# Kernel optimization log

Hardware: AMD Instinct MI355X
Metric: run time of the kernel (lower is better)

## Reference

```python
import jax, jax.numpy as jnp
import numpy as np

SIZE = 11
SIGMA = 1.5
ALPHA = 0.7
K1 = 0.01
K2 = 0.03
DATA_RANGE = 1.0
DN = ('NCDHW', 'OIDHW', 'NCDHW')


def _gauss1d():
    ax = jnp.arange(SIZE, dtype=jnp.float32) - SIZE // 2
    k = jnp.exp(-(ax ** 2) / (2.0 * SIGMA * SIGMA))
    return k / k.sum()


def _blur3d(x, k1):
    # Separable depthwise 3D gaussian blur with zero ('constant') padding.
    # Mathematically identical to the dense 11x11x11 outer-product conv3d
    # in the torch source (zero padding commutes with separable passes).
    ch = x.shape[1]
    pad = SIZE // 2
    for kshape in ((SIZE, 1, 1), (1, SIZE, 1), (1, 1, SIZE)):
        w = jnp.broadcast_to(k1.reshape(1, 1, *kshape), (ch, 1) + kshape)
        pads = [(pad, pad) if s == SIZE else (0, 0) for s in kshape]
        x = jax.lax.conv_general_dilated(
            x, w, window_strides=(1, 1, 1), padding=pads,
            dimension_numbers=DN, feature_group_count=ch)
    return x


def setup_inputs() -> dict:
    key = jax.random.key(0)
    k1, k2 = jax.random.split(key)
    shape = (2, 1, 160, 160, 160)
    pred = jax.random.uniform(k1, shape, dtype=jnp.float32)
    target = jax.random.uniform(k2, shape, dtype=jnp.float32)
    return {"pred": pred, "target": target}


def reference(pred, target):
    k1d = _gauss1d()
    pred32 = pred.astype(jnp.float32)
    target32 = target.astype(jnp.float32)

    # L1
    l1 = jnp.mean(jnp.abs(pred32 - target32))

    # SSIM3D
    mu1 = _blur3d(pred32, k1d)
    mu2 = _blur3d(target32, k1d)
    mu1_sq = mu1 * mu1
    mu2_sq = mu2 * mu2
    mu1_mu2 = mu1 * mu2
    sigma1_sq = _blur3d(pred32 * pred32, k1d) - mu1_sq
    sigma2_sq = _blur3d(target32 * target32, k1d) - mu2_sq
    sigma12 = _blur3d(pred32 * target32, k1d) - mu1_mu2

    C1 = (K1 * DATA_RANGE) ** 2
    C2 = (K2 * DATA_RANGE) ** 2
    ssim_map = ((2.0 * mu1_mu2 + C1) * (2.0 * sigma12 + C2)) / (
        (mu1_sq + mu2_sq + C1) * (sigma1_sq + sigma2_sq + C2) + 1e-12)
    ssim = jnp.mean(ssim_map)

    return ALPHA * l1 + (1.0 - ALPHA) * (1.0 - ssim)
```

## Files before the change

### kernel.cpp

```cpp
#include <hip/hip_runtime.h>

#define DHW 160
#define PLANE (160*160)
#define VOL (160*160*160)
#define PAD 5
#define KS 11
#define TXW 16
#define TYH 32
#define LZ 32
#define SRX 26
#define SRY 42
#define SRP 48
#define XBP 24
#define NSLOT 5
#define STAGE_NP (SRY*SRX)
#define NBLOCKS 500
#define CNT_POISON 0xAAAAAAAAu

__device__ __forceinline__ void gauss_w(float w[KS]) {
    float s = 0.f;
#pragma unroll
    for (int i = 0; i < KS; ++i) {
        float d = (float)(i - PAD);
        w[i] = expf(-(d * d) / (2.f * 1.5f * 1.5f));
        s += w[i];
    }
    float inv = 1.f / s;
#pragma unroll
    for (int i = 0; i < KS; ++i) w[i] *= inv;
}

__device__ __forceinline__ float block_reduce(float v, float* sm) {
#pragma unroll
    for (int off = 32; off > 0; off >>= 1)
        v += __shfl_down(v, off);
    int lane = threadIdx.x & 63;
    int wid  = threadIdx.x >> 6;
    if (lane == 0) sm[wid] = v;
    __syncthreads();
    float r = 0.f;
    if (threadIdx.x == 0) r = sm[0] + sm[1] + sm[2] + sm[3];
    return r;
}

__global__ __launch_bounds__(256, 2) void k_fused(
    const float* __restrict__ pred, const float* __restrict__ targ,
    double* __restrict__ accum, unsigned* __restrict__ cnt,
    float* __restrict__ out)
{
    __shared__ __align__(16) float sIn[2][SRY][SRP];
    __shared__ __align__(16) float sXB[5][SRY][XBP];
    __shared__ float sRed[4];

    float gw[KS]; gauss_w(gw);

    const int tile = blockIdx.x;
    const int xt = tile % 10, yt = tile / 10;
    const int z0 = blockIdx.y * LZ;
    const int b  = blockIdx.z;
    const float* __restrict__ P = pred + (size_t)b * VOL;
    const float* __restrict__ T = targ + (size_t)b * VOL;
    const ptrdiff_t dTP = T - P;

    const int tid = threadIdx.x;
    const int tx  = tid & 15;
    const int ty2 = tid >> 4;
    const int y0  = 2 * ty2;

    const float* sptrP[NSLOT];
    int  soff[NSLOT];
    bool sact[NSLOT];
    bool sl1[NSLOT];
#pragma unroll
    for (int i = 0; i < NSLOT; ++i) {
        int idx = tid + 256 * i;
        bool act = idx < STAGE_NP;
        int idc = act ? idx : 0;
        int r   = idc / SRX;
        int c   = idc - r * SRX;
        int gy = yt * TYH + r - PAD;
        int gx = xt * TXW + c - PAD;
        bool inp = (gy >= 0 && gy < DHW && gx >= 0 && gx < DHW);
        sact[i] = act && inp;
        sl1[i]  = act && (r >= PAD && r < PAD + TYH) && (c >= PAD && c < PAD + TXW);
        soff[i] = r * SRP + c;
        sptrP[i] = P + (inp ? (gy * DHW + gx) : 0);
    }

    auto stage_fetch = [&](int zz, float vp[NSLOT], float vt[NSLOT]) {
        bool zok = (zz >= 0 && zz < DHW);
        size_t zo = (size_t)(zok ? zz : 0) * PLANE;
#pragma unroll
        for (int i = 0; i < NSLOT; ++i) {
            bool ok = zok && sact[i];
            vp[i] = ok ? sptrP[i][zo] : 0.f;
            vt[i] = ok ? sptrP[i][zo + dTP] : 0.f;
        }
    };
    auto stage_write = [&](const float vp[NSLOT], const float vt[NSLOT]) {
        float* base = &sIn[0][0][0];
#pragma unroll
        for (int i = 0; i < NSLOT; ++i)
            if (tid + 256 * i < STAGE_NP) {
                base[soff[i]] = vp[i];
                base[SRY * SRP + soff[i]] = vt[i];
            }
    };

    float pend[2][5][KS];
#pragma unroll
    for (int o = 0; o < 2; ++o)
#pragma unroll
        for (int f = 0; f < 5; ++f)
#pragma unroll
            for (int j = 0; j < KS; ++j) pend[o][f][j] = 0.f;

    float l1s = 0.f, sss = 0.f;

    {
        float vp[NSLOT], vt[NSLOT];
        stage_fetch(z0 - PAD, vp, vt);
        stage_write(vp, vt);
    }
    __syncthreads();

    const int r4 = tid >> 2, cg = tid & 3;
    const bool xbAct = (tid < SRY * 4);

    const float C1 = 0.01f * 0.01f;
    const float C2 = 0.03f * 0.03f;

    for (int k = 0; k < LZ + 2 * PAD; ++k) {
        float pf_p[NSLOT], pf_t[NSLOT];
        const bool doStage = (k < LZ + 2 * PAD - 1);
        if (doStage) {
            stage_fetch(z0 - PAD + k + 1, pf_p, pf_t);
            if ((unsigned)(k + 1 - PAD) < (unsigned)LZ) {
#pragma unroll
                for (int i = 0; i < NSLOT; ++i)
                    if (sl1[i]) l1s += fabsf(pf_p[i] - pf_t[i]);
            }
        }

        if (xbAct) {
            const float4* rp = (const float4*)&sIn[0][r4][0];
            const float4* rt = (const float4*)&sIn[1][r4][0];
            float4 a0 = rp[cg], a1 = rp[cg + 1], a2 = rp[cg + 2], a3 = rp[cg + 3];
            float4 b0 = rt[cg], b1 = rt[cg + 1], b2 = rt[cg + 2], b3 = rt[cg + 3];
            float pv[16] = {a0.x,a0.y,a0.z,a0.w, a1.x,a1.y,a1.z,a1.w,
                            a2.x,a2.y,a2.z,a2.w, a3.x,a3.y,a3.z,a3.w};
            float tv[16] = {b0.x,b0.y,b0.z,b0.w, b1.x,b1.y,b1.z,b1.w,
                            b2.x,b2.y,b2.z,b2.w, b3.x,b3.y,b3.z,b3.w};
            float pp[14], tt2[14], pt2[14];
#pragma unroll
            for (int i = 0; i < 14; ++i) {
                pp[i]  = pv[i] * pv[i];
                tt2[i] = tv[i] * tv[i];
                pt2[i] = pv[i] * tv[i];
            }
            float o[5][4];
#pragma unroll
            for (int oo = 0; oo < 4; ++oo) {
                float s0 = 0, s1 = 0, s2 = 0, s3 = 0, s4 = 0;
#pragma unroll
                for (int j = 0; j < KS; ++j) {
                    float w = gw[j];
                    s0 += w * pv[oo + j];
                    s1 += w * tv[oo + j];
                    s2 += w * pp[oo + j];
                    s3 += w * tt2[oo + j];
                    s4 += w * pt2[oo + j];
                }
                o[0][oo] = s0; o[1][oo] = s1; o[2][oo] = s2;
                o[3][oo] = s3; o[4][oo] = s4;
            }
#pragma unroll
            for (int f = 0; f < 5; ++f) {
                float4 w4 = make_float4(o[f][0], o[f][1], o[f][2], o[f][3]);
                ((float4*)&sXB[f][r4][0])[cg] = w4;
            }
        }

        __syncthreads();

        if (doStage) stage_write(pf_p, pf_t);

        {
            float v[2][5];
#pragma unroll
            for (int f = 0; f < 5; ++f) {
                float tap[KS + 1];
#pragma unroll
                for (int j = 0; j < KS + 1; ++j)
                    tap[j] = sXB[f][y0 + j][tx];
                float a0 = 0.f, a1 = 0.f;
#pragma unroll
                for (int j = 0; j < KS; ++j) {
                    float w = gw[j];
                    a0 += w * tap[j];
                    a1 += w * tap[j + 1];
                }
                v[0][f] = a0;
                v[1][f] = a1;
            }
#pragma unroll
            for (int o = 0; o < 2; ++o) {
#pragma unroll
                for (int i = 0; i < KS - 1; ++i) {
                    float w = gw[10 - i];
#pragma unroll
                    for (int f = 0; f < 5; ++f)
                        pend[o][f][i] = pend[o][f][i + 1] + w * v[o][f];
                }
#pragma unroll
                for (int f = 0; f < 5; ++f)
                    pend[o][f][10] = gw[0] * v[o][f];
            }

            if (k >= 10) {
#pragma unroll
                for (int o = 0; o < 2; ++o) {
                    float m1 = pend[o][0][0], m2 = pend[o][1][0];
                    float e11 = pend[o][2][0], e22 = pend[o][3][0], e12 = pend[o][4][0];
                    float mu11 = m1 * m1, mu22 = m2 * m2, mu12 = m1 * m2;
                    float s1 = e11 - mu11, s2 = e22 - mu22, s12 = e12 - mu12;
                    float num = (2.f * mu12 + C1) * (2.f * s12 + C2);
                    float den = (mu11 + mu22 + C1) * (s1 + s2 + C2) + 1e-12f;
                    sss += num / den;
                }
            }
        }

        __syncthreads();
    }

    float r1 = block_reduce(l1s, sRed);
    __syncthreads();
    float r2 = block_reduce(sss, sRed);
    if (tid == 0) {
        atomicAdd(&accum[0], (double)r1);
        atomicAdd(&accum[1], (double)r2);
        __threadfence();
        unsigned prev = atomicAdd(cnt, 1u);
        if (prev == CNT_POISON + (unsigned)NBLOCKS - 1u) {
            const double n = 8192000.0;
            double l1   = atomicAdd(&accum[0], 0.0) / n;
            double ssim = atomicAdd(&accum[1], 0.0) / n;
            out[0] = (float)(0.7 * l1 + 0.3 * (1.0 - ssim));
        }
    }
}

extern "C" void kernel_launch(void* const* d_in, const int* in_sizes, int n_in,
                              void* d_out, int out_size, void* d_ws, size_t ws_size,
                              hipStream_t stream) {
    const float* pred = (const float*)d_in[0];
    const float* targ = (const float*)d_in[1];
    float* out = (float*)d_out;
    double* accum = (double*)d_ws;
    unsigned* cnt = (unsigned*)((char*)d_ws + 64);

    dim3 grid(50, DHW / LZ, 2);
    k_fused<<<grid, 256, 0, stream>>>(pred, targ, accum, cnt, out);
}
```

Before: 203.8 us.

## Process two z-slices per iteration to halve barrier count and balance x-blur work

The z loop now handles two slices per iteration, with double-sized shared buffers for the input staging and the x-blur results. All 256 threads now share the x-blur work (336 units spread over both slices, where before only 168 threads were active). This halves the number of __syncthreads per block and issues two slices of global loads at once. In exchange it raises register and shared memory pressure (the shared footprint roughly doubles), which may reduce occupancy below the 2 blocks per CU requested in the launch bounds.

```diff
diff --git a/kernel.cpp b/kernel.cpp
--- a/kernel.cpp
+++ b/kernel.cpp
@@ -14,6 +14,7 @@
 #define XBP 24
 #define NSLOT 5
 #define STAGE_NP (SRY*SRX)
+#define NITER ((LZ + 2*PAD) / 2)
 #define NBLOCKS 500
 #define CNT_POISON 0xAAAAAAAAu
 
@@ -48,8 +49,8 @@
     double* __restrict__ accum, unsigned* __restrict__ cnt,
     float* __restrict__ out)
 {
-    __shared__ __align__(16) float sIn[2][SRY][SRP];
-    __shared__ __align__(16) float sXB[5][SRY][XBP];
+    __shared__ __align__(16) float sIn[2][2][SRY][SRP];
+    __shared__ __align__(16) float sXB[2][5][SRY][XBP];
     __shared__ float sRed[4];
 
     float gw[KS]; gauss_w(gw);
@@ -97,14 +98,54 @@
             vt[i] = ok ? sptrP[i][zo + dTP] : 0.f;
         }
     };
-    auto stage_write = [&](const float vp[NSLOT], const float vt[NSLOT]) {
-        float* base = &sIn[0][0][0];
+    auto stage_write = [&](int slice, const float vp[NSLOT], const float vt[NSLOT]) {
+        float* basep = &sIn[slice][0][0][0];
+        float* baset = &sIn[slice][1][0][0];
 #pragma unroll
         for (int i = 0; i < NSLOT; ++i)
             if (tid + 256 * i < STAGE_NP) {
-                base[soff[i]] = vp[i];
-                base[SRY * SRP + soff[i]] = vt[i];
-            }
+                basep[soff[i]] = vp[i];
+                baset[soff[i]] = vt[i];
+            }
+    };
+
+    auto xblur_unit = [&](int s, int r4, int cg) {
+        const float4* rp = (const float4*)&sIn[s][0][r4][0];
+        const float4* rt = (const float4*)&sIn[s][1][r4][0];
+        float4 a0 = rp[cg], a1 = rp[cg + 1], a2 = rp[cg + 2], a3 = rp[cg + 3];
+        float4 b0 = rt[cg], b1 = rt[cg + 1], b2 = rt[cg + 2], b3 = rt[cg + 3];
+        float pv[16] = {a0.x,a0.y,a0.z,a0.w, a1.x,a1.y,a1.z,a1.w,
+                        a2.x,a2.y,a2.z,a2.w, a3.x,a3.y,a3.z,a3.w};
+        float tv[16] = {b0.x,b0.y,b0.z,b0.w, b1.x,b1.y,b1.z,b1.w,
+                        b2.x,b2.y,b2.z,b2.w, b3.x,b3.y,b3.z,b3.w};
+        float pp[14], tt2[14], pt2[14];
+#pragma unroll
+        for (int i = 0; i < 14; ++i) {
+            pp[i]  = pv[i] * pv[i];
+            tt2[i] = tv[i] * tv[i];
+            pt2[i] = pv[i] * tv[i];
+        }
+        float o[5][4];
+#pragma unroll
+        for (int oo = 0; oo < 4; ++oo) {
+            float s0 = 0, s1 = 0, s2 = 0, s3 = 0, s4 = 0;
+#pragma unroll
+            for (int j = 0; j < KS; ++j) {
+                float w = gw[j];
+                s0 += w * pv[oo + j];
+                s1 += w * tv[oo + j];
+                s2 += w * pp[oo + j];
+                s3 += w * tt2[oo + j];
+                s4 += w * pt2[oo + j];
+            }
+            o[0][oo] = s0; o[1][oo] = s1; o[2][oo] = s2;
+            o[3][oo] = s3; o[4][oo] = s4;
+        }
+#pragma unroll
+        for (int f = 0; f < 5; ++f) {
+            float4 w4 = make_float4(o[f][0], o[f][1], o[f][2], o[f][3]);
+            ((float4*)&sXB[s][f][r4][0])[cg] = w4;
+        }
     };
 
     float pend[2][5][KS];
@@ -116,120 +157,105 @@
             for (int j = 0; j < KS; ++j) pend[o][f][j] = 0.f;
 
     float l1s = 0.f, sss = 0.f;
+
+    const float C1 = 0.01f * 0.01f;
+    const float C2 = 0.03f * 0.03f;
+
+    auto yblur_push = [&](int s, bool doEmit) {
+        float v[2][5];
+#pragma unroll
+        for (int f = 0; f < 5; ++f) {
+            float tap[KS + 1];
+#pragma unroll
+            for (int j = 0; j < KS + 1; ++j)
+                tap[j] = sXB[s][f][y0 + j][tx];
+            float a0 = 0.f, a1 = 0.f;
+#pragma unroll
+            for (int j = 0; j < KS; ++j) {
+                float w = gw[j];
+                a0 += w * tap[j];
+                a1 += w * tap[j + 1];
+            }
+            v[0][f] = a0;
+            v[1][f] = a1;
+        }
+#pragma unroll
+        for (int o = 0; o < 2; ++o) {
+#pragma unroll
+            for (int i = 0; i < KS - 1; ++i) {
+                float w = gw[10 - i];
+#pragma unroll
+                for (int f = 0; f < 5; ++f)
+                    pend[o][f][i] = pend[o][f][i + 1] + w * v[o][f];
+            }
+#pragma unroll
+            for (int f = 0; f < 5; ++f)
+                pend[o][f][10] = gw[0] * v[o][f];
+        }
+        if (doEmit) {
+#pragma unroll
+            for (int o = 0; o < 2; ++o) {
+                float m1 = pend[o][0][0], m2 = pend[o][1][0];
+                float e11 = pend[o][2][0], e22 = pend[o][3][0], e12 = pend[o][4][0];
+                float mu11 = m1 * m1, mu22 = m2 * m2, mu12 = m1 * m2;
+                float s1 = e11 - mu11, s2 = e22 - mu22, s12 = e12 - mu12;
+                float num = (2.f * mu12 + C1) * (2.f * s12 + C2);
+                float den = (mu11 + mu22 + C1) * (s1 + s2 + C2) + 1e-12f;
+                sss += num / den;
+            }
+        }
+    };
 
     {
         float vp[NSLOT], vt[NSLOT];
         stage_fetch(z0 - PAD, vp, vt);
-        stage_write(vp, vt);
+        stage_write(0, vp, vt);
+        stage_fetch(z0 - PAD + 1, vp, vt);
+        stage_write(1, vp, vt);
     }
     __syncthreads();
 
-    const int r4 = tid >> 2, cg = tid & 3;
-    const bool xbAct = (tid < SRY * 4);
-
-    const float C1 = 0.01f * 0.01f;
-    const float C2 = 0.03f * 0.03f;
-
-    for (int k = 0; k < LZ + 2 * PAD; ++k) {
-        float pf_p[NSLOT], pf_t[NSLOT];
-        const bool doStage = (k < LZ + 2 * PAD - 1);
+    for (int m = 0; m < NITER; ++m) {
+        const int jA = 2 * m + 2, jB = 2 * m + 3;
+        float pA[NSLOT], tA[NSLOT], pB[NSLOT], tB[NSLOT];
+        const bool doStage = (m < NITER - 1);
+
         if (doStage) {
-            stage_fetch(z0 - PAD + k + 1, pf_p, pf_t);
-            if ((unsigned)(k + 1 - PAD) < (unsigned)LZ) {
+            stage_fetch(z0 - PAD + jA, pA, tA);
+            stage_fetch(z0 - PAD + jB, pB, tB);
+            if ((unsigned)(jA - PAD) < (unsigned)LZ) {
 #pragma unroll
                 for (int i = 0; i < NSLOT; ++i)
-                    if (sl1[i]) l1s += fabsf(pf_p[i] - pf_t[i]);
-            }
-        }
-
-        if (xbAct) {
-            const float4* rp = (const float4*)&sIn[0][r4][0];
-            const float4* rt = (const float4*)&sIn[1][r4][0];
-            float4 a0 = rp[cg], a1 = rp[cg + 1], a2 = rp[cg + 2], a3 = rp[cg + 3];
-            float4 b0 = rt[cg], b1 = rt[cg + 1], b2 = rt[cg + 2], b3 = rt[cg + 3];
-            float pv[16] = {a0.x,a0.y,a0.z,a0.w, a1.x,a1.y,a1.z,a1.w,
-                            a2.x,a2.y,a2.z,a2.w, a3.x,a3.y,a3.z,a3.w};
-            float tv[16] = {b0.x,b0.y,b0.z,b0.w, b1.x,b1.y,b1.z,b1.w,
-                            b2.x,b2.y,b2.z,b2.w, b3.x,b3.y,b3.z,b3.w};
-            float pp[14], tt2[14], pt2[14];
-#pragma unroll
-            for (int i = 0; i < 14; ++i) {
-                pp[i]  = pv[i] * pv[i];
-                tt2[i] = tv[i] * tv[i];
-                pt2[i] = pv[i] * tv[i];
-            }
-            float o[5][4];
-#pragma unroll
-            for (int oo = 0; oo < 4; ++oo) {
-                float s0 = 0, s1 = 0, s2 = 0, s3 = 0, s4 = 0;
-#pragma unroll
-                for (int j = 0; j < KS; ++j) {
-                    float w = gw[j];
-                    s0 += w * pv[oo + j];
-                    s1 += w * tv[oo + j];
-                    s2 += w * pp[oo + j];
-                    s3 += w * tt2[oo + j];
-                    s4 += w * pt2[oo + j];
-                }
-                o[0][oo] = s0; o[1][oo] = s1; o[2][oo] = s2;
-                o[3][oo] = s3; o[4][oo] = s4;
-            }
-#pragma unroll
-            for (int f = 0; f < 5; ++f) {
-                float4 w4 = make_float4(o[f][0], o[f][1], o[f][2], o[f][3]);
-                ((float4*)&sXB[f][r4][0])[cg] = w4;
+                    if (sl1[i]) l1s += fabsf(pA[i] - tA[i]);
+            }
+            if ((unsigned)(jB - PAD) < (unsigned)LZ) {
+#pragma unroll
+                for (int i = 0; i < NSLOT; ++i)
+                    if (sl1[i]) l1s += fabsf(pB[i] - tB[i]);
+            }
+        }
+
+        {
+            int u = tid;
+            int s = u / 168, rem = u - s * 168;
+            xblur_unit(s, rem >> 2, rem & 3);
+            if (tid < 336 - 256) {
+                int u2 = tid + 256;
+                int rem2 = u2 - 168;
+                xblur_unit(1, rem2 >> 2, rem2 & 3);
             }
         }
 
         __syncthreads();
 
-        if (doStage) stage_write(pf_p, pf_t);
-
-        {
-            float v[2][5];
-#pragma unroll
-            for (int f = 0; f < 5; ++f) {
-                float tap[KS + 1];
-#pragma unroll
-                for (int j = 0; j < KS + 1; ++j)
-                    tap[j] = sXB[f][y0 + j][tx];
-                float a0 = 0.f, a1 = 0.f;
-#pragma unroll
-                for (int j = 0; j < KS; ++j) {
-                    float w = gw[j];
-                    a0 += w * tap[j];
-                    a1 += w * tap[j + 1];
-                }
-                v[0][f] = a0;
-                v[1][f] = a1;
-            }
-#pragma unroll
-            for (int o = 0; o < 2; ++o) {
-#pragma unroll
-                for (int i = 0; i < KS - 1; ++i) {
-                    float w = gw[10 - i];
-#pragma unroll
-                    for (int f = 0; f < 5; ++f)
-                        pend[o][f][i] = pend[o][f][i + 1] + w * v[o][f];
-                }
-#pragma unroll
-                for (int f = 0; f < 5; ++f)
-                    pend[o][f][10] = gw[0] * v[o][f];
-            }
-
-            if (k >= 10) {
-#pragma unroll
-                for (int o = 0; o < 2; ++o) {
-                    float m1 = pend[o][0][0], m2 = pend[o][1][0];
-                    float e11 = pend[o][2][0], e22 = pend[o][3][0], e12 = pend[o][4][0];
-                    float mu11 = m1 * m1, mu22 = m2 * m2, mu12 = m1 * m2;
-                    float s1 = e11 - mu11, s2 = e22 - mu22, s12 = e12 - mu12;
-                    float num = (2.f * mu12 + C1) * (2.f * s12 + C2);
-                    float den = (mu11 + mu22 + C1) * (s1 + s2 + C2) + 1e-12f;
-                    sss += num / den;
-                }
-            }
-        }
+        if (doStage) {
+            stage_write(0, pA, tA);
+            stage_write(1, pB, tB);
+        }
+
+        const bool em = (m >= 5);
+        yblur_push(0, em);
+        yblur_push(1, em);
 
         __syncthreads();
     }
```

After: 198.4 us. -2.7%, faster.
